# Kernel optimization log

Hardware: AMD Instinct MI355X
Metric: run time of the kernel (lower is better)

Reference implementation:

```python
import jax, jax.numpy as jnp
import numpy as np

N_NODES = 100000
N_EDGES = 1600000
D = 128
LN_EPS = 1e-5


def setup_inputs() -> dict:
    key = jax.random.key(0)
    ks = jax.random.split(key, 6)
    return {
        "x": jax.random.normal(ks[0], (N_NODES, D), dtype=jnp.float32),
        "edge_src": jax.random.randint(ks[1], (N_EDGES,), 0, N_NODES, dtype=jnp.int32),
        "edge_dst": jax.random.randint(ks[2], (N_EDGES,), 0, N_NODES, dtype=jnp.int32),
        "edge_val": jax.random.uniform(ks[3], (N_EDGES,), dtype=jnp.float32),
        "w1": jax.random.normal(ks[4], (D,), dtype=jnp.float32),
        "w2": jax.random.normal(ks[5], (D,), dtype=jnp.float32),
        "ln1_g": jnp.ones((D,), dtype=jnp.float32),
        "ln1_b": jnp.zeros((D,), dtype=jnp.float32),
        "ln2_g": jnp.ones((D,), dtype=jnp.float32),
        "ln2_b": jnp.zeros((D,), dtype=jnp.float32),
    }


def _layer_norm(x, g, b):
    mu = jnp.mean(x, axis=-1, keepdims=True)
    var = jnp.mean(jnp.square(x - mu), axis=-1, keepdims=True)
    return (x - mu) * jax.lax.rsqrt(var + LN_EPS) * g + b


def _gat_layer(x, w, src, dst, val, g, b):
    # diag transform: h = x * w  (elementwise over features)
    h = x * w
    # sparse adjacency aggregation: out[dst] += val * h[src]
    msg = val[:, None] * h[src]  # [E, D]
    out = jax.ops.segment_sum(msg, dst, num_segments=x.shape[0])
    return _layer_norm(out, g, b)


def reference(x, edge_src, edge_dst, edge_val, w1, w2, ln1_g, ln1_b, ln2_g, ln2_b):
    # layer 0 (followed by ReLU; dropout is identity in eval mode)
    h = _gat_layer(x, w1, edge_src, edge_dst, edge_val, ln1_g, ln1_b)
    h = jax.nn.relu(h)
    # layer 1 (last layer: no ReLU/dropout)
    out = _gat_layer(h, w2, edge_src, edge_dst, edge_val, ln2_g, ln2_b)
    return out
```

## Files before the change

kernel.cpp:

```cpp
#include <hip/hip_runtime.h>

typedef __fp16 half2_t __attribute__((ext_vector_type(2)));

#define D 128
#define LN_EPS 1e-5f
#define BUCKET_NODES 128
#define BUCKET_SHIFT 7
#define EDGE_CAP 4096
#define FUSE_THREADS 512
#define K2_EPT 16
#define GT 1024

__device__ inline unsigned pack_h2(float a, float b) {
    half2_t p = __builtin_amdgcn_cvt_pkrtz(a, b);
    return __builtin_bit_cast(unsigned, p);
}

__global__ __launch_bounds__(FUSE_THREADS)
void conv_fill_kernel(const float* __restrict__ x, unsigned int* __restrict__ xb,
                      int nwords, int conv_blocks,
                      const int* __restrict__ src, const int* __restrict__ dst,
                      const float* __restrict__ val,
                      int* __restrict__ gcnt, uint2* __restrict__ edges,
                      int E, int nbuckets) {
    if ((int)blockIdx.x < conv_blocks) {
        int i = blockIdx.x * FUSE_THREADS + threadIdx.x;
        if (i < nwords) {
            int node = i >> 6, f = i & 63;
            xb[i] = pack_h2(x[(size_t)node * D + f], x[(size_t)node * D + 64 + f]);
        }
        return;
    }
    __shared__ int lcnt[1024];
    __shared__ int lbase[1024];
    int fb = (int)blockIdx.x - conv_blocks;
    for (int i = threadIdx.x; i < nbuckets; i += FUSE_THREADS) lcnt[i] = 0;
    __syncthreads();

    int base = fb * (FUSE_THREADS * K2_EPT);
    unsigned int w0[K2_EPT];
    float        w1[K2_EPT];
    int          br[K2_EPT];
    #pragma unroll
    for (int r = 0; r < K2_EPT; ++r) {
        int e = base + r * FUSE_THREADS + threadIdx.x;
        if (e < E) {
            int d = dst[e];
            int b = d >> BUCKET_SHIFT;
            int rk = atomicAdd(&lcnt[b], 1);
            w0[r] = (unsigned)src[e] | ((unsigned)(d & (BUCKET_NODES - 1)) << 20);
            w1[r] = val[e];
            br[r] = (b << 16) | rk;
        } else {
            br[r] = -1;
        }
    }
    __syncthreads();
    for (int i = threadIdx.x; i < nbuckets; i += FUSE_THREADS) {
        int c = lcnt[i];
        lbase[i] = c ? atomicAdd(&gcnt[i], c) : 0;
    }
    __syncthreads();
    #pragma unroll
    for (int r = 0; r < K2_EPT; ++r) {
        if (br[r] >= 0) {
            int b  = br[r] >> 16;
            int rk = br[r] & 0xffff;
            edges[(size_t)b * EDGE_CAP + lbase[b] + rk] =
                make_uint2(w0[r], __float_as_uint(w1[r]));
        }
    }
}

__global__ __launch_bounds__(GT, 8)
void gather_ln_kernel(const uint4* __restrict__ h4,
                      const int* __restrict__ gcnt,
                      const uint2* __restrict__ edges_g,
                      const float* __restrict__ w,
                      const float* __restrict__ g,
                      const float* __restrict__ bb,
                      float* __restrict__ out_f32,
                      unsigned int* __restrict__ out_h,
                      int N, int mode) {
    __shared__ uint2 eL[EDGE_CAP];
    __shared__ int hist[BUCKET_NODES];
    __shared__ int scanb[BUCKET_NODES];
    __shared__ int obase[BUCKET_NODES];

    int bkt = blockIdx.x;
    int tid = threadIdx.x;
    int cnt = min(gcnt[bkt], EDGE_CAP);
    const uint2* ep = edges_g + (size_t)bkt * EDGE_CAP;

    if (tid < BUCKET_NODES) hist[tid] = 0;
    __syncthreads();

    uint2 ed[4]; int dl[4]; int rk[4];
    #pragma unroll
    for (int r = 0; r < 4; ++r) {
        int i = r * GT + tid;
        if (i < cnt) {
            uint2 t = ep[i];
            ed[r] = t;
            dl[r] = (int)(t.x >> 20);
            rk[r] = atomicAdd(&hist[dl[r]], 1);
        } else dl[r] = -1;
    }
    __syncthreads();
    if (tid < BUCKET_NODES) scanb[tid] = hist[tid];
    __syncthreads();
    #pragma unroll
    for (int off = 1; off < BUCKET_NODES; off <<= 1) {
        int v = 0;
        if (tid < BUCKET_NODES && tid >= off) v = scanb[tid - off];
        __syncthreads();
        if (tid < BUCKET_NODES) scanb[tid] += v;
        __syncthreads();
    }
    if (tid < BUCKET_NODES) obase[tid] = scanb[tid] - hist[tid];
    __syncthreads();
    #pragma unroll
    for (int r = 0; r < 4; ++r)
        if (dl[r] >= 0) eL[obase[dl[r]] + rk[r]] = ed[r];
    __syncthreads();

    int wid = tid >> 6, lane = tid & 63, grp = lane >> 4, sl = lane & 15;

    float4 wA = ((const float4*)w)[sl];
    float4 wB = ((const float4*)(w + 64))[sl];
    float4 gA = ((const float4*)g)[sl];
    float4 gB = ((const float4*)(g + 64))[sl];
    float4 bA = ((const float4*)bb)[sl];
    float4 bB = ((const float4*)(bb + 64))[sl];

    #pragma unroll
    for (int k = 0; k < 2; ++k) {
        int ni = k * 64 + wid * 4 + grp;
        int n = (bkt << BUCKET_SHIFT) + ni;
        if (n >= N) continue;
        int st = obase[ni], m = hist[ni];

        float aA0=0,aA1=0,aA2=0,aA3=0, aB0=0,aB1=0,aB2=0,aB3=0;
        for (int j = 0; j < m; j += 2) {
            uint2 tA = eL[st + j];
            uint2 tB = (j + 1 < m) ? eL[st + j + 1] : make_uint2(0u, 0u);
            int   sA = (int)(tA.x & 0xfffffu);
            float vA = __uint_as_float(tA.y);
            int   sB = (int)(tB.x & 0xfffffu);
            float vB = __uint_as_float(tB.y);
            uint4 hA = h4[(size_t)sA * 16 + sl];
            uint4 hB = h4[(size_t)sB * 16 + sl];
            half2_t p;
            p = __builtin_bit_cast(half2_t, hA.x);
            aA0 = fmaf(vA, (float)p.x, aA0); aB0 = fmaf(vA, (float)p.y, aB0);
            p = __builtin_bit_cast(half2_t, hA.y);
            aA1 = fmaf(vA, (float)p.x, aA1); aB1 = fmaf(vA, (float)p.y, aB1);
            p = __builtin_bit_cast(half2_t, hA.z);
            aA2 = fmaf(vA, (float)p.x, aA2); aB2 = fmaf(vA, (float)p.y, aB2);
            p = __builtin_bit_cast(half2_t, hA.w);
            aA3 = fmaf(vA, (float)p.x, aA3); aB3 = fmaf(vA, (float)p.y, aB3);
            p = __builtin_bit_cast(half2_t, hB.x);
            aA0 = fmaf(vB, (float)p.x, aA0); aB0 = fmaf(vB, (float)p.y, aB0);
            p = __builtin_bit_cast(half2_t, hB.y);
            aA1 = fmaf(vB, (float)p.x, aA1); aB1 = fmaf(vB, (float)p.y, aB1);
            p = __builtin_bit_cast(half2_t, hB.z);
            aA2 = fmaf(vB, (float)p.x, aA2); aB2 = fmaf(vB, (float)p.y, aB2);
            p = __builtin_bit_cast(half2_t, hB.w);
            aA3 = fmaf(vB, (float)p.x, aA3); aB3 = fmaf(vB, (float)p.y, aB3);
        }

        aA0 *= wA.x; aA1 *= wA.y; aA2 *= wA.z; aA3 *= wA.w;
        aB0 *= wB.x; aB1 *= wB.y; aB2 *= wB.z; aB3 *= wB.w;

        float sum = ((aA0 + aA1) + (aA2 + aA3)) + ((aB0 + aB1) + (aB2 + aB3));
        sum += __shfl_xor(sum, 1, 64); sum += __shfl_xor(sum, 2, 64);
        sum += __shfl_xor(sum, 4, 64); sum += __shfl_xor(sum, 8, 64);
        float mu = sum * (1.0f / D);

        float dA0 = aA0 - mu, dA1 = aA1 - mu, dA2 = aA2 - mu, dA3 = aA3 - mu;
        float dB0 = aB0 - mu, dB1 = aB1 - mu, dB2 = aB2 - mu, dB3 = aB3 - mu;
        float sq = ((dA0*dA0 + dA1*dA1) + (dA2*dA2 + dA3*dA3))
                 + ((dB0*dB0 + dB1*dB1) + (dB2*dB2 + dB3*dB3));
        sq += __shfl_xor(sq, 1, 64); sq += __shfl_xor(sq, 2, 64);
        sq += __shfl_xor(sq, 4, 64); sq += __shfl_xor(sq, 8, 64);
        float rstd = rsqrtf(sq * (1.0f / D) + LN_EPS);

        float oA0 = dA0 * rstd * gA.x + bA.x, oA1 = dA1 * rstd * gA.y + bA.y;
        float oA2 = dA2 * rstd * gA.z + bA.z, oA3 = dA3 * rstd * gA.w + bA.w;
        float oB0 = dB0 * rstd * gB.x + bB.x, oB1 = dB1 * rstd * gB.y + bB.y;
        float oB2 = dB2 * rstd * gB.z + bB.z, oB3 = dB3 * rstd * gB.w + bB.w;

        if (mode == 1) {
            oA0 = fmaxf(oA0, 0.f); oA1 = fmaxf(oA1, 0.f);
            oA2 = fmaxf(oA2, 0.f); oA3 = fmaxf(oA3, 0.f);
            oB0 = fmaxf(oB0, 0.f); oB1 = fmaxf(oB1, 0.f);
            oB2 = fmaxf(oB2, 0.f); oB3 = fmaxf(oB3, 0.f);
            uint4 pw;
            pw.x = pack_h2(oA0, oB0); pw.y = pack_h2(oA1, oB1);
            pw.z = pack_h2(oA2, oB2); pw.w = pack_h2(oA3, oB3);
            ((uint4*)(out_h + (size_t)n * 64))[sl] = pw;
        } else {
            ((float4*)(out_f32 + (size_t)n * D))[sl]      = make_float4(oA0, oA1, oA2, oA3);
            ((float4*)(out_f32 + (size_t)n * D + 64))[sl] = make_float4(oB0, oB1, oB2, oB3);
        }
    }
}

extern "C" void kernel_launch(void* const* d_in, const int* in_sizes, int n_in,
                              void* d_out, int out_size, void* d_ws, size_t ws_size,
                              hipStream_t stream) {
    const float* x    = (const float*)d_in[0];
    const int*   esrc = (const int*)d_in[1];
    const int*   edst = (const int*)d_in[2];
    const float* eval_= (const float*)d_in[3];
    const float* w1   = (const float*)d_in[4];
    const float* w2   = (const float*)d_in[5];
    const float* g1   = (const float*)d_in[6];
    const float* b1   = (const float*)d_in[7];
    const float* g2   = (const float*)d_in[8];
    const float* b2   = (const float*)d_in[9];
    float* out = (float*)d_out;

    const int N = in_sizes[0] / D;
    const int E = in_sizes[1];
    const int nbuckets = (N + BUCKET_NODES - 1) >> BUCKET_SHIFT;

    unsigned int* xb    = (unsigned int*)d_ws;
    unsigned int* hb    = xb + (size_t)N * 64;
    uint2*        edges = (uint2*)(hb + (size_t)N * 64);
    int*          gcnt  = (int*)(edges + (size_t)nbuckets * EDGE_CAP);

    const int nwords = N * 64;
    const int conv_blocks = (nwords + FUSE_THREADS - 1) / FUSE_THREADS;
    const int fill_blocks = (E + FUSE_THREADS * K2_EPT - 1) / (FUSE_THREADS * K2_EPT);

    (void)hipMemsetAsync(gcnt, 0, (size_t)nbuckets * sizeof(int), stream);
    conv_fill_kernel<<<conv_blocks + fill_blocks, FUSE_THREADS, 0, stream>>>(
        x, xb, nwords, conv_blocks, esrc, edst, eval_, gcnt, edges, E, nbuckets);
    gather_ln_kernel<<<nbuckets, GT, 0, stream>>>((const uint4*)xb, gcnt, edges,
                                                  w1, g1, b1, nullptr, hb, N, 1);
    gather_ln_kernel<<<nbuckets, GT, 0, stream>>>((const uint4*)hb, gcnt, edges,
                                                  w2, g2, b2, out, nullptr, N, 0);
}
```

Baseline: 292.5 us.

## Halve gather block size, unroll edge gather by four, defer param loads

Shrinks the gather/LayerNorm block from 1024 to 512 threads, so each thread loads 8 edges and each wave processes 4 node passes instead of 2. Edge placement now uses an atomic cursor per destination node instead of keeping per-edge ranks in registers. The inner gather loop issues four independent row loads per iteration instead of two, and the w/g/b parameter loads move inside the node loop next to where they are used. The aim is more memory-level parallelism and lower register pressure. In exchange, each wave handles its nodes serially over more passes, and edge order within a node, and so float summation order, can change between runs.

```diff
diff --git a/kernel.cpp b/kernel.cpp
--- a/kernel.cpp
+++ b/kernel.cpp
@@ -9,7 +9,7 @@
 #define EDGE_CAP 4096
 #define FUSE_THREADS 512
 #define K2_EPT 16
-#define GT 1024
+#define GT 512
 
 __device__ inline unsigned pack_h2(float a, float b) {
     half2_t p = __builtin_amdgcn_cvt_pkrtz(a, b);
@@ -86,6 +86,7 @@
     __shared__ int hist[BUCKET_NODES];
     __shared__ int scanb[BUCKET_NODES];
     __shared__ int obase[BUCKET_NODES];
+    __shared__ int place[BUCKET_NODES];
 
     int bkt = blockIdx.x;
     int tid = threadIdx.x;
@@ -95,16 +96,15 @@
     if (tid < BUCKET_NODES) hist[tid] = 0;
     __syncthreads();
 
-    uint2 ed[4]; int dl[4]; int rk[4];
-    #pragma unroll
-    for (int r = 0; r < 4; ++r) {
+    uint2 ed[8];
+    #pragma unroll
+    for (int r = 0; r < 8; ++r) {
         int i = r * GT + tid;
         if (i < cnt) {
             uint2 t = ep[i];
             ed[r] = t;
-            dl[r] = (int)(t.x >> 20);
-            rk[r] = atomicAdd(&hist[dl[r]], 1);
-        } else dl[r] = -1;
+            atomicAdd(&hist[(int)(t.x >> 20)], 1);
+        }
     }
     __syncthreads();
     if (tid < BUCKET_NODES) scanb[tid] = hist[tid];
@@ -117,58 +117,72 @@
         if (tid < BUCKET_NODES) scanb[tid] += v;
         __syncthreads();
     }
-    if (tid < BUCKET_NODES) obase[tid] = scanb[tid] - hist[tid];
-    __syncthreads();
-    #pragma unroll
-    for (int r = 0; r < 4; ++r)
-        if (dl[r] >= 0) eL[obase[dl[r]] + rk[r]] = ed[r];
+    if (tid < BUCKET_NODES) {
+        int ob = scanb[tid] - hist[tid];
+        obase[tid] = ob;
+        place[tid] = ob;
+    }
+    __syncthreads();
+    #pragma unroll
+    for (int r = 0; r < 8; ++r) {
+        int i = r * GT + tid;
+        if (i < cnt) {
+            int b = (int)(ed[r].x >> 20);
+            int pos = atomicAdd(&place[b], 1);
+            eL[pos] = ed[r];
+        }
+    }
     __syncthreads();
 
     int wid = tid >> 6, lane = tid & 63, grp = lane >> 4, sl = lane & 15;
 
-    float4 wA = ((const float4*)w)[sl];
-    float4 wB = ((const float4*)(w + 64))[sl];
-    float4 gA = ((const float4*)g)[sl];
-    float4 gB = ((const float4*)(g + 64))[sl];
-    float4 bA = ((const float4*)bb)[sl];
-    float4 bB = ((const float4*)(bb + 64))[sl];
-
-    #pragma unroll
-    for (int k = 0; k < 2; ++k) {
-        int ni = k * 64 + wid * 4 + grp;
+    #pragma unroll 1
+    for (int k = 0; k < 4; ++k) {
+        int ni = k * 32 + wid * 4 + grp;
         int n = (bkt << BUCKET_SHIFT) + ni;
         if (n >= N) continue;
         int st = obase[ni], m = hist[ni];
 
         float aA0=0,aA1=0,aA2=0,aA3=0, aB0=0,aB1=0,aB2=0,aB3=0;
-        for (int j = 0; j < m; j += 2) {
-            uint2 tA = eL[st + j];
-            uint2 tB = (j + 1 < m) ? eL[st + j + 1] : make_uint2(0u, 0u);
-            int   sA = (int)(tA.x & 0xfffffu);
-            float vA = __uint_as_float(tA.y);
-            int   sB = (int)(tB.x & 0xfffffu);
-            float vB = __uint_as_float(tB.y);
-            uint4 hA = h4[(size_t)sA * 16 + sl];
-            uint4 hB = h4[(size_t)sB * 16 + sl];
-            half2_t p;
-            p = __builtin_bit_cast(half2_t, hA.x);
-            aA0 = fmaf(vA, (float)p.x, aA0); aB0 = fmaf(vA, (float)p.y, aB0);
-            p = __builtin_bit_cast(half2_t, hA.y);
-            aA1 = fmaf(vA, (float)p.x, aA1); aB1 = fmaf(vA, (float)p.y, aB1);
-            p = __builtin_bit_cast(half2_t, hA.z);
-            aA2 = fmaf(vA, (float)p.x, aA2); aB2 = fmaf(vA, (float)p.y, aB2);
-            p = __builtin_bit_cast(half2_t, hA.w);
-            aA3 = fmaf(vA, (float)p.x, aA3); aB3 = fmaf(vA, (float)p.y, aB3);
-            p = __builtin_bit_cast(half2_t, hB.x);
-            aA0 = fmaf(vB, (float)p.x, aA0); aB0 = fmaf(vB, (float)p.y, aB0);
-            p = __builtin_bit_cast(half2_t, hB.y);
-            aA1 = fmaf(vB, (float)p.x, aA1); aB1 = fmaf(vB, (float)p.y, aB1);
-            p = __builtin_bit_cast(half2_t, hB.z);
-            aA2 = fmaf(vB, (float)p.x, aA2); aB2 = fmaf(vB, (float)p.y, aB2);
-            p = __builtin_bit_cast(half2_t, hB.w);
-            aA3 = fmaf(vB, (float)p.x, aA3); aB3 = fmaf(vB, (float)p.y, aB3);
-        }
-
+
+        #define ACC(H, V)                                                      \
+            {   half2_t p;                                                     \
+                p = __builtin_bit_cast(half2_t, (H).x);                        \
+                aA0 = fmaf((V), (float)p.x, aA0); aB0 = fmaf((V), (float)p.y, aB0); \
+                p = __builtin_bit_cast(half2_t, (H).y);                        \
+                aA1 = fmaf((V), (float)p.x, aA1); aB1 = fmaf((V), (float)p.y, aB1); \
+                p = __builtin_bit_cast(half2_t, (H).z);                        \
+                aA2 = fmaf((V), (float)p.x, aA2); aB2 = fmaf((V), (float)p.y, aB2); \
+                p = __builtin_bit_cast(half2_t, (H).w);                        \
+                aA3 = fmaf((V), (float)p.x, aA3); aB3 = fmaf((V), (float)p.y, aB3); }
+
+        int m4 = m & ~3;
+        int j = 0;
+        for (; j < m4; j += 4) {
+            uint2 t0 = eL[st + j];
+            uint2 t1 = eL[st + j + 1];
+            uint2 t2 = eL[st + j + 2];
+            uint2 t3 = eL[st + j + 3];
+            uint4 h0 = h4[(size_t)(t0.x & 0xfffffu) * 16 + sl];
+            uint4 h1 = h4[(size_t)(t1.x & 0xfffffu) * 16 + sl];
+            uint4 h2 = h4[(size_t)(t2.x & 0xfffffu) * 16 + sl];
+            uint4 h3 = h4[(size_t)(t3.x & 0xfffffu) * 16 + sl];
+            float v0 = __uint_as_float(t0.y);
+            float v1 = __uint_as_float(t1.y);
+            float v2 = __uint_as_float(t2.y);
+            float v3 = __uint_as_float(t3.y);
+            ACC(h0, v0); ACC(h1, v1); ACC(h2, v2); ACC(h3, v3);
+        }
+        for (; j < m; ++j) {
+            uint2 t0 = eL[st + j];
+            uint4 h0 = h4[(size_t)(t0.x & 0xfffffu) * 16 + sl];
+            float v0 = __uint_as_float(t0.y);
+            ACC(h0, v0);
+        }
+        #undef ACC
+
+        float4 wA = ((const float4*)w)[sl];
+        float4 wB = ((const float4*)(w + 64))[sl];
         aA0 *= wA.x; aA1 *= wA.y; aA2 *= wA.z; aA3 *= wA.w;
         aB0 *= wB.x; aB1 *= wB.y; aB2 *= wB.z; aB3 *= wB.w;
 
@@ -184,6 +198,11 @@
         sq += __shfl_xor(sq, 1, 64); sq += __shfl_xor(sq, 2, 64);
         sq += __shfl_xor(sq, 4, 64); sq += __shfl_xor(sq, 8, 64);
         float rstd = rsqrtf(sq * (1.0f / D) + LN_EPS);
+
+        float4 gA = ((const float4*)g)[sl];
+        float4 gB = ((const float4*)(g + 64))[sl];
+        float4 bA = ((const float4*)bb)[sl];
+        float4 bB = ((const float4*)(bb + 64))[sl];
 
         float oA0 = dA0 * rstd * gA.x + bA.x, oA1 = dA1 * rstd * gA.y + bA.y;
         float oA2 = dA2 * rstd * gA.z + bA.z, oA3 = dA3 * rstd * gA.w + bA.w;
```

New measurement: 292.9 us. No clear change (+0.1%).
